# Optimization experiments

Measured on AMD Instinct MI355X. Metric: run time of the kernel, lower is better.

The kernel has to match this reference:

```python
import jax, jax.numpy as jnp
import numpy as np

B, T, D, H = 4, 2048, 1024, 16
HD = D // H


def setup_inputs() -> dict:
    key = jax.random.key(0)
    ks = jax.random.split(key, 6)
    s = 0.02
    return {
        "x": jax.random.normal(ks[0], (B, T, D), dtype=jnp.float32),
        "padding_mask": jnp.zeros((B, T), dtype=bool),
        "Wq": jax.random.normal(ks[1], (D, D), dtype=jnp.float32) * s,
        "Wk": jax.random.normal(ks[2], (D, D), dtype=jnp.float32) * s,
        "Wv": jax.random.normal(ks[3], (D, D), dtype=jnp.float32) * s,
        "Wo": jax.random.normal(ks[4], (D, D), dtype=jnp.float32) * s,
        "bo": jax.random.normal(ks[5], (D,), dtype=jnp.float32) * s,
    }


def reference(x, padding_mask, Wq, Wk, Wv, Wo, bo):
    # torch nn.Linear: y = x @ W.T
    b, t, d = x.shape
    q = (x @ Wq.T).reshape(b, t, H, HD).transpose(0, 2, 1, 3)  # [B,H,T,hd]
    k = (x @ Wk.T).reshape(b, t, H, HD).transpose(0, 2, 1, 3)
    v = (x @ Wv.T).reshape(b, t, H, HD).transpose(0, 2, 1, 3)

    scores = jnp.einsum("bhid,bhjd->bhij", q, k) / jnp.sqrt(jnp.float32(HD))
    causal = jnp.tril(jnp.ones((t, t), dtype=bool))  # [T,T]
    neg_inf = jnp.float32(-jnp.inf)
    scores = jnp.where(causal[None, None, :, :], scores, neg_inf)
    scores = jnp.where(padding_mask[:, None, None, :], neg_inf, scores)

    attn = jax.nn.softmax(scores, axis=-1)
    out = jnp.einsum("bhij,bhjd->bhid", attn, v)
    out = out.transpose(0, 2, 1, 3).reshape(b, t, d)
    out = out @ Wo.T + bo
    nonpad = (~padding_mask)[:, :, None].astype(out.dtype)
    return out * nonpad
```

## Files before the change

### kernel.cpp

```cpp
#include <hip/hip_runtime.h>

#define B_ 4
#define T_ 2048
#define D_ 1024
#define H_ 16
#define BT_ (B_ * T_)
#define QSCALE (0.125f * 1.44269504088896f)

typedef unsigned short u16;
typedef unsigned long long u64;
typedef __attribute__((ext_vector_type(8))) __bf16 bf16x8;
typedef __attribute__((ext_vector_type(4))) float f32x4;

__device__ __forceinline__ u16 f2bf(float f) {
  unsigned u = __builtin_bit_cast(unsigned, f);
  u += 0x7FFFu + ((u >> 16) & 1u);
  return (u16)(u >> 16);
}

__device__ __forceinline__ void gload16(const void* g, void* l) {
  __builtin_amdgcn_global_load_lds(
      (const __attribute__((address_space(1))) void*)g,
      (__attribute__((address_space(3))) void*)l, 16, 0, 0);
}

__global__ void cvt_bf16(const float* __restrict__ in, u16* __restrict__ out, int n4) {
  int i = blockIdx.x * 256 + threadIdx.x;
  if (i >= n4) return;
  const float4 v = ((const float4*)in)[i];
  ushort4 o;
  o.x = f2bf(v.x); o.y = f2bf(v.y); o.z = f2bf(v.z); o.w = f2bf(v.w);
  ((ushort4*)out)[i] = o;
}

__global__ void cvt_wts(const float* __restrict__ Wq, const float* __restrict__ Wk,
                        const float* __restrict__ Wv, const float* __restrict__ Wo,
                        u16* __restrict__ wdst,
                        const unsigned char* __restrict__ pm, unsigned char* __restrict__ fl) {
  const int by = blockIdx.y;
  if (by < 4) {
    const float* src = (by == 0) ? Wq : (by == 1) ? Wk : (by == 2) ? Wv : Wo;
    const int i = blockIdx.x * 256 + threadIdx.x;
    const float4 v = ((const float4*)src)[i];
    ushort4 o;
    o.x = f2bf(v.x); o.y = f2bf(v.y); o.z = f2bf(v.z); o.w = f2bf(v.w);
    ((ushort4*)(wdst + (size_t)by * D_ * D_))[i] = o;
  } else if (blockIdx.x == 0 && threadIdx.x < 128) {
    const int i = threadIdx.x;
    const unsigned long long* p = (const unsigned long long*)(pm + i * 64);
    unsigned long long acc = 0;
#pragma unroll
    for (int k = 0; k < 8; ++k) acc |= p[k];
    fl[i] = acc ? 1 : 0;
  }
}

template<int MODE>
__global__ __launch_bounds__(256, 2) void gemm_bt(
    const u16* __restrict__ A, const u16* __restrict__ Bw,
    float* __restrict__ Cf, const float* __restrict__ bias,
    const unsigned char* __restrict__ rowmask,
    u16* __restrict__ Cq, u16* __restrict__ Ck, u16* __restrict__ Cvt)
{
  __shared__ __align__(16) u16 sA[128 * 64];
  __shared__ __align__(16) u16 sB[128 * 64];
  const int tid = threadIdx.x;
  const int lane = tid & 63, wave = tid >> 6;
  const int g = lane >> 4, s15 = lane & 15;
  const int bm = blockIdx.x * 128, bn = blockIdx.y * 128;
  const int wr = wave >> 1, wc = wave & 1;

  const int srow = lane >> 3;
  const int scol = ((lane & 7) ^ srow) << 3;

  f32x4 acc[4][4] = {};

  for (int kt = 0; kt < 16; ++kt) {
    __syncthreads();
    const int k0 = kt << 6;
#pragma unroll
    for (int c = 0; c < 4; ++c) {
      const int chunk = c * 4 + wave;
      gload16(A  + (size_t)(bm + chunk * 8 + srow) * 1024 + k0 + scol, (char*)sA + chunk * 1024);
      gload16(Bw + (size_t)(bn + chunk * 8 + srow) * 1024 + k0 + scol, (char*)sB + chunk * 1024);
    }
    __syncthreads();
#pragma unroll
    for (int kk = 0; kk < 2; ++kk) {
      const int cb = ((kk << 6) | (g << 4)) ^ ((s15 & 7) << 4);
      bf16x8 af[4], bf[4];
#pragma unroll
      for (int mm = 0; mm < 4; ++mm)
        af[mm] = *(const bf16x8*)((const char*)sA + (wr * 64 + mm * 16 + s15) * 128 + cb);
#pragma unroll
      for (int nn = 0; nn < 4; ++nn)
        bf[nn] = *(const bf16x8*)((const char*)sB + (wc * 64 + nn * 16 + s15) * 128 + cb);
#pragma unroll
      for (int mm = 0; mm < 4; ++mm)
#pragma unroll
        for (int nn = 0; nn < 4; ++nn)
          acc[mm][nn] = __builtin_amdgcn_mfma_f32_16x16x32_bf16(af[mm], bf[nn], acc[mm][nn], 0, 0, 0);
    }
  }

  if (MODE == 1) {
    const int region = bn >> 10;
    const float a = (region == 0) ? QSCALE : 1.f;
#pragma unroll
    for (int mm = 0; mm < 4; ++mm)
#pragma unroll
      for (int nn = 0; nn < 4; ++nn) {
        const int col = bn + wc * 64 + nn * 16 + s15;
        const int colr = col & 1023;
        const int row0 = bm + wr * 64 + mm * 16 + (g << 2);
        if (region == 2) {
          ushort4 w;
          w.x = f2bf(acc[mm][nn][0]); w.y = f2bf(acc[mm][nn][1]);
          w.z = f2bf(acc[mm][nn][2]); w.w = f2bf(acc[mm][nn][3]);
          *(ushort4*)(Cvt + (size_t)colr * BT_ + row0) = w;
        } else {
          u16* dst = region ? Ck : Cq;
#pragma unroll
          for (int r = 0; r < 4; ++r)
            dst[(size_t)(row0 + r) * 1024 + colr] = f2bf(acc[mm][nn][r] * a);
        }
      }
  } else {
#pragma unroll
    for (int mm = 0; mm < 4; ++mm)
#pragma unroll
      for (int nn = 0; nn < 4; ++nn) {
        const int col = bn + wc * 64 + nn * 16 + s15;
        const int row0 = bm + wr * 64 + mm * 16 + (g << 2);
        const float bv = bias[col];
#pragma unroll
        for (int r = 0; r < 4; ++r) {
          float v = acc[mm][nn][r] + bv;
          v = rowmask[row0 + r] ? 0.f : v;
          Cf[(size_t)(row0 + r) * 1024 + col] = v;
        }
      }
  }
}

__global__ __launch_bounds__(512, 4) void attn_fwd(
    const u16* __restrict__ Q, const u16* __restrict__ K,
    const u16* __restrict__ VT, const unsigned char* __restrict__ pm,
    const unsigned char* __restrict__ tileflag, u16* __restrict__ O)
{
  __shared__ __align__(16) u16 sK[3][64 * 64];
  __shared__ __align__(16) u16 sV[3][64 * 64];
  const int tid = threadIdx.x;
  const int lane = tid & 63, wave = tid >> 6;
  const int g = lane >> 4, s15 = lane & 15;
  const int bh = blockIdx.x, b = bh >> 4, h = bh & 15;
  const int j = blockIdx.y;
  const size_t tokbase = (size_t)b * T_;

  const int qw0 = j * 128 + wave * 16;
  const int qw1 = (15 - j) * 128 + wave * 16;
  const int nt = 32 - 2 * j;

  const int srow = tid >> 3;
  const int sc = (tid & 7) ^ (srow & 7);
  const u16* Kb0 = K + tokbase * D_ + h * 64 + sc * 8;
  const u16* Vb0 = VT + (size_t)(h * 64) * BT_ + tokbase + sc * 8;

  u64 flq[4];
#pragma unroll
  for (int q = 0; q < 4; ++q) flq[q] = ((const u64*)(tileflag + b * 32))[q];

  bf16x8 qf[2][2];
#pragma unroll
  for (int ks = 0; ks < 2; ++ks) {
    qf[0][ks] = *(const bf16x8*)(Q + (tokbase + qw0 + s15) * D_ + h * 64 + ks * 32 + g * 8);
    qf[1][ks] = *(const bf16x8*)(Q + (tokbase + qw1 + s15) * D_ + h * 64 + ks * 32 + g * 8);
  }

  f32x4 o[2][4] = {};
  f32x4 l4[2] = {};

  gload16(Kb0 + (size_t)srow * D_,        (char*)(&sK[0][0]) + tid * 16);
  gload16(Vb0 + (size_t)srow * BT_,       (char*)(&sV[0][0]) + tid * 16);
  gload16(Kb0 + (size_t)(64 + srow) * D_, (char*)(&sK[1][0]) + tid * 16);
  gload16(Vb0 + (size_t)srow * BT_ + 64,  (char*)(&sV[1][0]) + tid * 16);
  asm volatile("s_waitcnt vmcnt(2) lgkmcnt(0)" ::: "memory");
  __builtin_amdgcn_s_barrier();
  asm volatile("" ::: "memory");

  int rd = 0, st2 = 2;
  for (int t = 0; t < nt; ++t) {
    const int kv0 = t << 6;
    if (t + 2 < nt) {
      gload16(Kb0 + (size_t)(kv0 + 128 + srow) * D_, (char*)(&sK[st2][0]) + tid * 16);
      gload16(Vb0 + (size_t)srow * BT_ + kv0 + 128,  (char*)(&sV[st2][0]) + tid * 16);
    }

    const bool act0 = (kv0 <= qw0 + 15);
    const bool act1 = (kv0 <= qw1 + 15);
    const u16* kb_ = &sK[rd][0];
    const u16* vb_ = &sV[rd][0];

    f32x4 st[4][2] = {};
#pragma unroll
    for (int ks = 0; ks < 2; ++ks) {
      bf16x8 kf[4];
#pragma unroll
      for (int jf = 0; jf < 4; ++jf)
        kf[jf] = *(const bf16x8*)(kb_ + (jf * 16 + s15) * 64 + (((ks * 4 + g) ^ (s15 & 7)) << 3));
      __builtin_amdgcn_s_setprio(1);
      if (act0)
#pragma unroll
        for (int jf = 0; jf < 4; ++jf)
          st[jf][0] = __builtin_amdgcn_mfma_f32_16x16x32_bf16(kf[jf], qf[0][ks], st[jf][0], 0, 0, 0);
      if (act1)
#pragma unroll
        for (int jf = 0; jf < 4; ++jf)
          st[jf][1] = __builtin_amdgcn_mfma_f32_16x16x32_bf16(kf[jf], qf[1][ks], st[jf][1], 0, 0, 0);
      __builtin_amdgcn_s_setprio(0);
    }

    if (act0 && kv0 + 63 > qw0) {
      const int iq = qw0 + s15;
#pragma unroll
      for (int jf = 0; jf < 4; ++jf) {
        const int jb = kv0 + jf * 16 + g * 4;
#pragma unroll
        for (int r = 0; r < 4; ++r)
          if (jb + r > iq) st[jf][0][r] = -1e30f;
      }
    }
    if (act1 && kv0 + 63 > qw1) {
      const int iq = qw1 + s15;
#pragma unroll
      for (int jf = 0; jf < 4; ++jf) {
        const int jb = kv0 + jf * 16 + g * 4;
#pragma unroll
        for (int r = 0; r < 4; ++r)
          if (jb + r > iq) st[jf][1][r] = -1e30f;
      }
    }
    if ((flq[t >> 3] >> ((t & 7) * 8)) & 0xff) {
#pragma unroll
      for (int jf = 0; jf < 4; ++jf) {
        const int jb = kv0 + jf * 16 + g * 4;
        uchar4 p4 = *(const uchar4*)(pm + b * T_ + jb);
        const unsigned char* pr = (const unsigned char*)&p4;
#pragma unroll
        for (int r = 0; r < 4; ++r)
          if (pr[r]) { st[jf][0][r] = -1e30f; st[jf][1][r] = -1e30f; }
      }
    }

    if (act0)
#pragma unroll
      for (int jf = 0; jf < 4; ++jf) {
#pragma unroll
        for (int r = 0; r < 4; ++r)
          st[jf][0][r] = __builtin_amdgcn_exp2f(st[jf][0][r]);
        l4[0] += st[jf][0];
      }
    if (act1)
#pragma unroll
      for (int jf = 0; jf < 4; ++jf) {
#pragma unroll
        for (int r = 0; r < 4; ++r)
          st[jf][1][r] = __builtin_amdgcn_exp2f(st[jf][1][r]);
        l4[1] += st[jf][1];
      }

#pragma unroll
    for (int kb2 = 0; kb2 < 2; ++kb2) {
      bf16x8 vf[4];
#pragma unroll
      for (int df = 0; df < 4; ++df)
        vf[df] = *(const bf16x8*)(vb_ + (df * 16 + s15) * 64 + (((kb2 * 4 + g) ^ (s15 & 7)) << 3));
#pragma unroll
      for (int nf = 0; nf < 2; ++nf) {
        if (nf == 0 ? !act0 : !act1) continue;
        unsigned w00, w01, w10, w11;
        asm("v_cvt_pk_bf16_f32 %0, %1, %2" : "=v"(w00) : "v"(st[2*kb2][nf][0]),   "v"(st[2*kb2][nf][1]));
        asm("v_cvt_pk_bf16_f32 %0, %1, %2" : "=v"(w01) : "v"(st[2*kb2][nf][2]),   "v"(st[2*kb2][nf][3]));
        asm("v_cvt_pk_bf16_f32 %0, %1, %2" : "=v"(w10) : "v"(st[2*kb2+1][nf][0]), "v"(st[2*kb2+1][nf][1]));
        asm("v_cvt_pk_bf16_f32 %0, %1, %2" : "=v"(w11) : "v"(st[2*kb2+1][nf][2]), "v"(st[2*kb2+1][nf][3]));
        asm("v_permlane32_swap_b32 %0, %1" : "+v"(w00), "+v"(w10));
        asm("v_permlane16_swap_b32 %0, %1" : "+v"(w00), "+v"(w10));
        asm("v_permlane32_swap_b32 %0, %1" : "+v"(w01), "+v"(w11));
        asm("v_permlane16_swap_b32 %0, %1" : "+v"(w01), "+v"(w11));
        union { unsigned u[4]; bf16x8 v; } pf;
        pf.u[0] = w00; pf.u[1] = w01; pf.u[2] = w10; pf.u[3] = w11;
        __builtin_amdgcn_s_setprio(1);
#pragma unroll
        for (int df = 0; df < 4; ++df)
          o[nf][df] = __builtin_amdgcn_mfma_f32_16x16x32_bf16(vf[df], pf.v, o[nf][df], 0, 0, 0);
        __builtin_amdgcn_s_setprio(0);
      }
    }

    if (t + 1 < nt) {
      if (t + 2 < nt) asm volatile("s_waitcnt vmcnt(2) lgkmcnt(0)" ::: "memory");
      else            asm volatile("s_waitcnt vmcnt(0) lgkmcnt(0)" ::: "memory");
      __builtin_amdgcn_s_barrier();
      asm volatile("" ::: "memory");
    }
    rd  = (rd  == 2) ? 0 : rd + 1;
    st2 = (st2 == 2) ? 0 : st2 + 1;
  }

#pragma unroll
  for (int nf = 0; nf < 2; ++nf) {
    float lv = (l4[nf][0] + l4[nf][1]) + (l4[nf][2] + l4[nf][3]);
    lv += __shfl_xor(lv, 16);
    lv += __shfl_xor(lv, 32);
    const float inv = 1.f / lv;
    const int qw = nf ? qw1 : qw0;
    u16* orow = O + (tokbase + qw + s15) * D_ + h * 64 + g * 4;
#pragma unroll
    for (int df = 0; df < 4; ++df) {
      ushort4 w;
      w.x = f2bf(o[nf][df][0] * inv); w.y = f2bf(o[nf][df][1] * inv);
      w.z = f2bf(o[nf][df][2] * inv); w.w = f2bf(o[nf][df][3] * inv);
      *(ushort4*)(orow + df * 16) = w;
    }
  }
}

extern "C" void kernel_launch(void* const* d_in, const int* in_sizes, int n_in,
                              void* d_out, int out_size, void* d_ws, size_t ws_size,
                              hipStream_t stream)
{
  const float* x  = (const float*)d_in[0];
  const unsigned char* pm = (const unsigned char*)d_in[1];
  const float* Wq = (const float*)d_in[2];
  const float* Wk = (const float*)d_in[3];
  const float* Wv = (const float*)d_in[4];
  const float* Wo = (const float*)d_in[5];
  const float* bo = (const float*)d_in[6];
  float* out = (float*)d_out;

  char* w = (char*)d_ws;
  u16* xb  = (u16*)w; w += (size_t)BT_ * D_ * 2;
  u16* wqb = (u16*)w; w += (size_t)D_ * D_ * 2;
  u16* wkb = (u16*)w; w += (size_t)D_ * D_ * 2;
  u16* wvb = (u16*)w; w += (size_t)D_ * D_ * 2;
  u16* wob = (u16*)w; w += (size_t)D_ * D_ * 2;
  u16* qb  = (u16*)w; w += (size_t)BT_ * D_ * 2;
  u16* kbf = (u16*)w; w += (size_t)BT_ * D_ * 2;
  u16* vt  = (u16*)w; w += (size_t)BT_ * D_ * 2;
  u16* ao  = (u16*)w; w += (size_t)BT_ * D_ * 2;
  unsigned char* flags = (unsigned char*)w; w += 256;
  (void)wkb; (void)wvb;

  const int nx4 = BT_ * D_ / 4;
  cvt_bf16<<<nx4 / 256, 256, 0, stream>>>(x, xb, nx4);
  cvt_wts<<<dim3(1024, 5), 256, 0, stream>>>(Wq, Wk, Wv, Wo, wqb, pm, flags);

  gemm_bt<1><<<dim3(64, 24), 256, 0, stream>>>(xb, wqb, nullptr, nullptr, nullptr, qb, kbf, vt);

  attn_fwd<<<dim3(B_ * H_, 8), 512, 0, stream>>>(qb, kbf, vt, pm, flags, ao);

  gemm_bt<0><<<dim3(64, 8), 256, 0, stream>>>(ao, wob, out, bo, pm, nullptr, nullptr, nullptr);
}
```

Before: 142.1 us.

## Software-pipeline QK of next tile with softmax/PV and deepen KV ring to 4

Restructures the attention inner loop so the QK^T MFMAs for tile t+1 are issued before the masking, exp2 and PV work of tile t. Two score buffers alternate, and the loop is unrolled by two. The K/V LDS ring grows from 3 to 4 stages, with prefetch three tiles ahead. The aim is to overlap MFMA work with the VALU exp2 work and to hide global load latency better. In exchange, LDS use and register pressure go up, which may lower occupancy.

```diff
diff --git a/kernel.cpp b/kernel.cpp
--- a/kernel.cpp
+++ b/kernel.cpp
@@ -148,8 +148,8 @@
     const u16* __restrict__ VT, const unsigned char* __restrict__ pm,
     const unsigned char* __restrict__ tileflag, u16* __restrict__ O)
 {
-  __shared__ __align__(16) u16 sK[3][64 * 64];
-  __shared__ __align__(16) u16 sV[3][64 * 64];
+  __shared__ __align__(16) u16 sK[4][64 * 64];
+  __shared__ __align__(16) u16 sV[4][64 * 64];
   const int tid = threadIdx.x;
   const int lane = tid & 63, wave = tid >> 6;
   const int g = lane >> 4, s15 = lane & 15;
@@ -180,28 +180,21 @@
   f32x4 o[2][4] = {};
   f32x4 l4[2] = {};
 
-  gload16(Kb0 + (size_t)srow * D_,        (char*)(&sK[0][0]) + tid * 16);
-  gload16(Vb0 + (size_t)srow * BT_,       (char*)(&sV[0][0]) + tid * 16);
-  gload16(Kb0 + (size_t)(64 + srow) * D_, (char*)(&sK[1][0]) + tid * 16);
-  gload16(Vb0 + (size_t)srow * BT_ + 64,  (char*)(&sV[1][0]) + tid * 16);
+#pragma unroll
+  for (int s = 0; s < 3; ++s) {
+    gload16(Kb0 + (size_t)(s * 64 + srow) * D_,   (char*)(&sK[s][0]) + tid * 16);
+    gload16(Vb0 + (size_t)srow * BT_ + s * 64,    (char*)(&sV[s][0]) + tid * 16);
+  }
   asm volatile("s_waitcnt vmcnt(2) lgkmcnt(0)" ::: "memory");
   __builtin_amdgcn_s_barrier();
   asm volatile("" ::: "memory");
 
-  int rd = 0, st2 = 2;
-  for (int t = 0; t < nt; ++t) {
+  auto QK = [&](int t, f32x4 (&st)[4][2]) {
     const int kv0 = t << 6;
-    if (t + 2 < nt) {
-      gload16(Kb0 + (size_t)(kv0 + 128 + srow) * D_, (char*)(&sK[st2][0]) + tid * 16);
-      gload16(Vb0 + (size_t)srow * BT_ + kv0 + 128,  (char*)(&sV[st2][0]) + tid * 16);
-    }
-
-    const bool act0 = (kv0 <= qw0 + 15);
-    const bool act1 = (kv0 <= qw1 + 15);
-    const u16* kb_ = &sK[rd][0];
-    const u16* vb_ = &sV[rd][0];
-
-    f32x4 st[4][2] = {};
+    const bool a0 = (kv0 <= qw0 + 15), a1 = (kv0 <= qw1 + 15);
+    const u16* kb_ = &sK[t & 3][0];
+#pragma unroll
+    for (int jf = 0; jf < 4; ++jf) { st[jf][0] = f32x4{}; st[jf][1] = f32x4{}; }
 #pragma unroll
     for (int ks = 0; ks < 2; ++ks) {
       bf16x8 kf[4];
@@ -209,35 +202,47 @@
       for (int jf = 0; jf < 4; ++jf)
         kf[jf] = *(const bf16x8*)(kb_ + (jf * 16 + s15) * 64 + (((ks * 4 + g) ^ (s15 & 7)) << 3));
       __builtin_amdgcn_s_setprio(1);
-      if (act0)
+      if (a0)
 #pragma unroll
         for (int jf = 0; jf < 4; ++jf)
           st[jf][0] = __builtin_amdgcn_mfma_f32_16x16x32_bf16(kf[jf], qf[0][ks], st[jf][0], 0, 0, 0);
-      if (act1)
+      if (a1)
 #pragma unroll
         for (int jf = 0; jf < 4; ++jf)
           st[jf][1] = __builtin_amdgcn_mfma_f32_16x16x32_bf16(kf[jf], qf[1][ks], st[jf][1], 0, 0, 0);
       __builtin_amdgcn_s_setprio(0);
     }
-
-    if (act0 && kv0 + 63 > qw0) {
+  };
+
+  auto ITER = [&](int t, f32x4 (&cur)[4][2], f32x4 (&nxt)[4][2]) {
+    const int kv0 = t << 6;
+    if (t + 3 < nt) {
+      const int s = (t + 3) & 3;
+      gload16(Kb0 + (size_t)(kv0 + 192 + srow) * D_, (char*)(&sK[s][0]) + tid * 16);
+      gload16(Vb0 + (size_t)srow * BT_ + kv0 + 192,  (char*)(&sV[s][0]) + tid * 16);
+    }
+    if (t + 1 < nt) QK(t + 1, nxt);
+
+    const bool a0 = (kv0 <= qw0 + 15), a1 = (kv0 <= qw1 + 15);
+
+    if (a0 && kv0 + 63 > qw0) {
       const int iq = qw0 + s15;
 #pragma unroll
       for (int jf = 0; jf < 4; ++jf) {
         const int jb = kv0 + jf * 16 + g * 4;
 #pragma unroll
         for (int r = 0; r < 4; ++r)
-          if (jb + r > iq) st[jf][0][r] = -1e30f;
-      }
-    }
-    if (act1 && kv0 + 63 > qw1) {
+          if (jb + r > iq) cur[jf][0][r] = -1e30f;
+      }
+    }
+    if (a1 && kv0 + 63 > qw1) {
       const int iq = qw1 + s15;
 #pragma unroll
       for (int jf = 0; jf < 4; ++jf) {
         const int jb = kv0 + jf * 16 + g * 4;
 #pragma unroll
         for (int r = 0; r < 4; ++r)
-          if (jb + r > iq) st[jf][1][r] = -1e30f;
+          if (jb + r > iq) cur[jf][1][r] = -1e30f;
       }
     }
     if ((flq[t >> 3] >> ((t & 7) * 8)) & 0xff) {
@@ -248,27 +253,28 @@
         const unsigned char* pr = (const unsigned char*)&p4;
 #pragma unroll
         for (int r = 0; r < 4; ++r)
-          if (pr[r]) { st[jf][0][r] = -1e30f; st[jf][1][r] = -1e30f; }
-      }
-    }
-
-    if (act0)
-#pragma unroll
-      for (int jf = 0; jf < 4; ++jf) {
-#pragma unroll
-        for (int r = 0; r < 4; ++r)
-          st[jf][0][r] = __builtin_amdgcn_exp2f(st[jf][0][r]);
-        l4[0] += st[jf][0];
-      }
-    if (act1)
-#pragma unroll
-      for (int jf = 0; jf < 4; ++jf) {
-#pragma unroll
-        for (int r = 0; r < 4; ++r)
-          st[jf][1][r] = __builtin_amdgcn_exp2f(st[jf][1][r]);
-        l4[1] += st[jf][1];
-      }
-
+          if (pr[r]) { cur[jf][0][r] = -1e30f; cur[jf][1][r] = -1e30f; }
+      }
+    }
+
+    if (a0)
+#pragma unroll
+      for (int jf = 0; jf < 4; ++jf) {
+#pragma unroll
+        for (int r = 0; r < 4; ++r)
+          cur[jf][0][r] = __builtin_amdgcn_exp2f(cur[jf][0][r]);
+        l4[0] += cur[jf][0];
+      }
+    if (a1)
+#pragma unroll
+      for (int jf = 0; jf < 4; ++jf) {
+#pragma unroll
+        for (int r = 0; r < 4; ++r)
+          cur[jf][1][r] = __builtin_amdgcn_exp2f(cur[jf][1][r]);
+        l4[1] += cur[jf][1];
+      }
+
+    const u16* vb_ = &sV[t & 3][0];
 #pragma unroll
     for (int kb2 = 0; kb2 < 2; ++kb2) {
       bf16x8 vf[4];
@@ -277,12 +283,12 @@
         vf[df] = *(const bf16x8*)(vb_ + (df * 16 + s15) * 64 + (((kb2 * 4 + g) ^ (s15 & 7)) << 3));
 #pragma unroll
       for (int nf = 0; nf < 2; ++nf) {
-        if (nf == 0 ? !act0 : !act1) continue;
+        if (nf == 0 ? !a0 : !a1) continue;
         unsigned w00, w01, w10, w11;
-        asm("v_cvt_pk_bf16_f32 %0, %1, %2" : "=v"(w00) : "v"(st[2*kb2][nf][0]),   "v"(st[2*kb2][nf][1]));
-        asm("v_cvt_pk_bf16_f32 %0, %1, %2" : "=v"(w01) : "v"(st[2*kb2][nf][2]),   "v"(st[2*kb2][nf][3]));
-        asm("v_cvt_pk_bf16_f32 %0, %1, %2" : "=v"(w10) : "v"(st[2*kb2+1][nf][0]), "v"(st[2*kb2+1][nf][1]));
-        asm("v_cvt_pk_bf16_f32 %0, %1, %2" : "=v"(w11) : "v"(st[2*kb2+1][nf][2]), "v"(st[2*kb2+1][nf][3]));
+        asm("v_cvt_pk_bf16_f32 %0, %1, %2" : "=v"(w00) : "v"(cur[2*kb2][nf][0]),   "v"(cur[2*kb2][nf][1]));
+        asm("v_cvt_pk_bf16_f32 %0, %1, %2" : "=v"(w01) : "v"(cur[2*kb2][nf][2]),   "v"(cur[2*kb2][nf][3]));
+        asm("v_cvt_pk_bf16_f32 %0, %1, %2" : "=v"(w10) : "v"(cur[2*kb2+1][nf][0]), "v"(cur[2*kb2+1][nf][1]));
+        asm("v_cvt_pk_bf16_f32 %0, %1, %2" : "=v"(w11) : "v"(cur[2*kb2+1][nf][2]), "v"(cur[2*kb2+1][nf][3]));
         asm("v_permlane32_swap_b32 %0, %1" : "+v"(w00), "+v"(w10));
         asm("v_permlane16_swap_b32 %0, %1" : "+v"(w00), "+v"(w10));
         asm("v_permlane32_swap_b32 %0, %1" : "+v"(w01), "+v"(w11));
@@ -298,13 +304,19 @@
     }
 
     if (t + 1 < nt) {
-      if (t + 2 < nt) asm volatile("s_waitcnt vmcnt(2) lgkmcnt(0)" ::: "memory");
+      if (t + 3 < nt) asm volatile("s_waitcnt vmcnt(2) lgkmcnt(0)" ::: "memory");
       else            asm volatile("s_waitcnt vmcnt(0) lgkmcnt(0)" ::: "memory");
       __builtin_amdgcn_s_barrier();
       asm volatile("" ::: "memory");
     }
-    rd  = (rd  == 2) ? 0 : rd + 1;
-    st2 = (st2 == 2) ? 0 : st2 + 1;
+  };
+
+  f32x4 stA[4][2], stB[4][2];
+  QK(0, stA);
+
+  for (int t = 0; t < nt; t += 2) {
+    ITER(t, stA, stB);
+    ITER(t + 1, stB, stA);
   }
 
 #pragma unroll
```

New measurement: 564.1 us (median of 2 runs). 297% more time.
